# Kernel tuning notes

Measured on AMD Instinct MI355X. Metric: run time of the kernel, lower is better.

## Reference

```python
import jax, jax.numpy as jnp
import numpy as np

N = 50000   # nodes
E = 640000  # edges
D_IN = 128
D_OUT = 128
EPS = 1e-5


def _layer_norm(x, gamma, beta):
    mu = jnp.mean(x, axis=-1, keepdims=True)
    var = jnp.mean(jnp.square(x - mu), axis=-1, keepdims=True)
    return (x - mu) * jax.lax.rsqrt(var + EPS) * gamma + beta


def _sage_conv(x, src, dst, w_l, b_l, w_r):
    # PyG SAGEConv (aggr='mean', root_weight=True, normalize=False):
    #   out = lin_l(mean_{j in N(i)} x_j) + lin_r(x_i)
    msgs = x[src]                                             # [E, D]
    agg = jax.ops.segment_sum(msgs, dst, num_segments=N)      # [N, D]
    cnt = jax.ops.segment_sum(jnp.ones((E,), x.dtype), dst, num_segments=N)
    mean = agg / jnp.maximum(cnt, 1.0)[:, None]
    return mean @ w_l.T + b_l + x @ w_r.T


def setup_inputs() -> dict:
    key = jax.random.key(0)
    ks = jax.random.split(key, 12)
    s_in = 1.0 / np.sqrt(D_IN)
    s_out = 1.0 / np.sqrt(D_OUT)
    return {
        "x": jax.random.normal(ks[0], (N, D_IN), jnp.float32),
        "edges": jax.random.randint(ks[1], (2, E), 0, N),
        "dp_w": jax.random.uniform(ks[2], (D_OUT, D_IN), jnp.float32, -s_in, s_in),
        "dp_b": jnp.zeros((D_OUT,), jnp.float32),
        "sc_w": jax.random.uniform(ks[3], (D_OUT, D_IN), jnp.float32, -s_in, s_in),
        "sc_b": jnp.zeros((D_OUT,), jnp.float32),
        "g1_lw": jax.random.uniform(ks[4], (D_OUT, D_OUT), jnp.float32, -s_out, s_out),
        "g1_lb": jnp.zeros((D_OUT,), jnp.float32),
        "g1_rw": jax.random.uniform(ks[5], (D_OUT, D_OUT), jnp.float32, -s_out, s_out),
        "n1_g": jnp.ones((D_OUT,), jnp.float32),
        "n1_b": jnp.zeros((D_OUT,), jnp.float32),
        "g2_lw": jax.random.uniform(ks[6], (D_OUT, D_OUT), jnp.float32, -s_out, s_out),
        "g2_lb": jnp.zeros((D_OUT,), jnp.float32),
        "g2_rw": jax.random.uniform(ks[7], (D_OUT, D_OUT), jnp.float32, -s_out, s_out),
        "n2_g": jnp.ones((D_OUT,), jnp.float32),
        "n2_b": jnp.zeros((D_OUT,), jnp.float32),
    }


def reference(x, edges, dp_w, dp_b, sc_w, sc_b, g1_lw, g1_lb, g1_rw, n1_g, n1_b,
              g2_lw, g2_lb, g2_rw, n2_g, n2_b):
    gelu = lambda v: jax.nn.gelu(v, approximate=False)
    src, dst = edges[0], edges[1]
    shortcut = x @ sc_w.T + sc_b
    h = gelu(x @ dp_w.T + dp_b)
    h = _sage_conv(h, src, dst, g1_lw, g1_lb, g1_rw)
    h = gelu(_layer_norm(h, n1_g, n1_b))
    h = _sage_conv(h, src, dst, g2_lw, g2_lb, g2_rw)
    h = _layer_norm(h, n2_g, n2_b)
    return gelu(h + shortcut)
```

## Files before the change

kernel.cpp:

```cpp
#include <hip/hip_runtime.h>
#include <hip/hip_bf16.h>
#include <math.h>

#define D 128
#define WS 136
#define FS 132
#define PB 128

typedef __attribute__((ext_vector_type(8))) short bf16x8;
typedef __attribute__((ext_vector_type(4))) float f32x4;

__device__ __forceinline__ unsigned short f2bf(float f){
  return (unsigned short)((__float_as_uint(f) + 0x8000u) >> 16);
}
__device__ __forceinline__ float bf2f(unsigned short h){
  return __uint_as_float(((unsigned)h) << 16);
}
__device__ __forceinline__ float bf2f_lo(unsigned v){
  return __uint_as_float(v << 16);
}
__device__ __forceinline__ float bf2f_hi(unsigned v){
  return __uint_as_float(v & 0xFFFF0000u);
}
__device__ __forceinline__ float gelu_fast(float v){
  float u = v * v;
  float arg = v * (1.5957691216f + 0.0713548163f * u);
  arg = fminf(arg, 60.0f);
  float e = __expf(arg);
  return v * e * __builtin_amdgcn_rcpf(e + 1.0f);
}

__global__ __launch_bounds__(256) void k_prepcnt(const float* s0, const float* s1,
    const float* s2, const float* s3, const float* s4, const float* s5,
    unsigned short* dst, const int* __restrict__ edst, int* __restrict__ cnt,
    int E, int nbuck, int epb){
  __shared__ int hist[512];
  if (blockIdx.x < 48){
    int gt = blockIdx.x * 256 + threadIdx.x;
    int m = gt >> 11;
    int r = gt & 2047;
    int f = r >> 6, lane = r & 63;
    int t = f & 7, kk = f >> 3;
    int row = t * 16 + (lane & 15);
    int col = kk * 32 + (lane >> 4) * 8;
    const float* src;
    if (m == 0) src = s0; else if (m == 1) src = s1; else if (m == 2) src = s2;
    else if (m == 3) src = s3; else if (m == 4) src = s4; else src = s5;
    src += row * 128 + col;
    float4 a = *(const float4*)src;
    float4 bb = *(const float4*)(src + 4);
    bf16x8 o;
    o[0] = (short)f2bf(a.x);  o[1] = (short)f2bf(a.y);
    o[2] = (short)f2bf(a.z);  o[3] = (short)f2bf(a.w);
    o[4] = (short)f2bf(bb.x); o[5] = (short)f2bf(bb.y);
    o[6] = (short)f2bf(bb.z); o[7] = (short)f2bf(bb.w);
    int pair = m >> 1, half = m & 1;
    *(bf16x8*)(dst + (size_t)pair * 32768 + (((size_t)f * 2 + half) * 64 + lane) * 8) = o;
    return;
  }
  int blk = blockIdx.x - 48;
  for (int b = threadIdx.x; b < nbuck; b += 256) hist[b] = 0;
  __syncthreads();
  int start = blk * epb;
  int end = min(E, start + epb);
  for (int e = start + threadIdx.x; e < end; e += 256)
    atomicAdd(&hist[edst[e] >> 7], 1);
  __syncthreads();
  for (int b = threadIdx.x; b < nbuck; b += 256) cnt[blk * nbuck + b] = hist[b];
}

__global__ __launch_bounds__(256) void k_pscan(const int* __restrict__ cnt,
    int* __restrict__ offs, int* __restrict__ bbase, int E, int nbuck){
  __shared__ int tot[512], base[512];
  int t = threadIdx.x;
  for (int b = t; b < nbuck; b += 256){
    int s = 0;
    for (int blk = 0; blk < PB; blk++) s += cnt[blk * nbuck + b];
    tot[b] = s;
  }
  __syncthreads();
  for (int b = t; b < nbuck; b += 256){
    int s = 0;
    for (int j = 0; j < b; j++) s += tot[j];
    base[b] = s;
  }
  __syncthreads();
  for (int b = t; b < nbuck; b += 256){
    bbase[b] = base[b];
    int run = base[b];
    for (int blk = 0; blk < PB; blk++){
      offs[blk * nbuck + b] = run;
      run += cnt[blk * nbuck + b];
    }
  }
  if (t == 0) bbase[nbuck] = E;
}

__global__ __launch_bounds__(256) void k_pscatter(const int* __restrict__ esrc,
    const int* __restrict__ edst, const int* __restrict__ offs,
    unsigned* __restrict__ ebuf, int E, int nbuck, int epb){
  __shared__ int loff[512];
  for (int b = threadIdx.x; b < nbuck; b += 256) loff[b] = offs[blockIdx.x * nbuck + b];
  __syncthreads();
  int start = blockIdx.x * epb;
  int end = min(E, start + epb);
  for (int e = start + threadIdx.x; e < end; e += 256){
    int s = esrc[e], d = edst[e];
    int b = d >> 7;
    int pos = atomicAdd(&loff[b], 1);
    ebuf[pos] = (unsigned)s | ((unsigned)(d & 127) << 16);
  }
}

__global__ __launch_bounds__(256) void k_csrin(
    const unsigned* __restrict__ ebuf, const int* __restrict__ bbase,
    int* __restrict__ off, int* __restrict__ csr,
    const float* __restrict__ x, const unsigned short* __restrict__ wp,
    const float* __restrict__ scb, const float* __restrict__ dpb,
    unsigned short* __restrict__ sbuf, unsigned short* __restrict__ hbuf,
    int N, int E, int nbuck){
  __shared__ int cnt[128], pref[128], curs[128];
  __shared__ unsigned short tile[64 * WS];
  int tid = threadIdx.x;
  if ((int)blockIdx.x < nbuck){
    int b = blockIdx.x;
    int start = bbase[b], end = bbase[b + 1];
    if (tid < 128) cnt[tid] = 0;
    __syncthreads();
    for (int e = start + tid; e < end; e += 256)
      atomicAdd(&cnt[ebuf[e] >> 16], 1);
    __syncthreads();
    if (tid < 128) pref[tid] = cnt[tid];
    __syncthreads();
    for (int ofs = 1; ofs < 128; ofs <<= 1){
      int v = 0;
      if (tid < 128 && tid >= ofs) v = pref[tid - ofs];
      __syncthreads();
      if (tid < 128) pref[tid] += v;
      __syncthreads();
    }
    if (tid < 128){
      int ex = pref[tid] - cnt[tid];
      curs[tid] = ex;
      int node = b * 128 + tid;
      if (node < N) off[node] = start + ex;
    }
    if (b == 0 && tid == 0) off[N] = E;
    __syncthreads();
    for (int e = start + tid; e < end; e += 256){
      unsigned u = ebuf[e];
      int d = u >> 16;
      int p = atomicAdd(&curs[d], 1);
      csr[start + p] = (int)(u & 0xFFFFu);
    }
    return;
  }
  int bx = blockIdx.x - nbuck;
  int w = tid >> 6, lane = tid & 63, quad = lane >> 4, l16 = lane & 15;
  int nbb = bx * 64;
  int nb = nbb + w * 16;
  int arow = min(nb + l16, N - 1);
  f32x4 acc[2][8];
  #pragma unroll
  for (int m = 0; m < 2; m++)
    #pragma unroll
    for (int t = 0; t < 8; t++) acc[m][t] = (f32x4){0.f, 0.f, 0.f, 0.f};
  #pragma unroll
  for (int kk = 0; kk < 4; kk++){
    const float* xp = x + (size_t)arow * D + kk * 32 + quad * 8;
    float4 xa = *(const float4*)xp;
    float4 xb = *(const float4*)(xp + 4);
    bf16x8 a;
    a[0] = (short)f2bf(xa.x); a[1] = (short)f2bf(xa.y);
    a[2] = (short)f2bf(xa.z); a[3] = (short)f2bf(xa.w);
    a[4] = (short)f2bf(xb.x); a[5] = (short)f2bf(xb.y);
    a[6] = (short)f2bf(xb.z); a[7] = (short)f2bf(xb.w);
    #pragma unroll
    for (int t = 0; t < 8; t++){
      size_t fo = (((size_t)(kk * 8 + t) * 2) * 64 + lane) * 8;
      bf16x8 b0 = *(const bf16x8*)(wp + fo);
      bf16x8 b1 = *(const bf16x8*)(wp + fo + 512);
      acc[0][t] = __builtin_amdgcn_mfma_f32_16x16x32_bf16(a, b0, acc[0][t], 0, 0, 0);
      acc[1][t] = __builtin_amdgcn_mfma_f32_16x16x32_bf16(a, b1, acc[1][t], 0, 0, 0);
    }
  }
  #pragma unroll
  for (int m = 0; m < 2; m++){
    const float* bias = m ? dpb : scb;
    #pragma unroll
    for (int t = 0; t < 8; t++){
      float bv = bias[t * 16 + l16];
      #pragma unroll
      for (int r = 0; r < 4; r++){
        int nl = w * 16 + quad * 4 + r;
        float v = acc[m][t][r] + bv;
        if (m) v = gelu_fast(v);
        tile[nl * WS + t * 16 + l16] = f2bf(v);
      }
    }
    __syncthreads();
    unsigned short* dst = m ? hbuf : sbuf;
    #pragma unroll
    for (int i = 0; i < 4; i++){
      int c = tid + 256 * i;
      int nl = c >> 4, j = c & 15;
      int node = nbb + nl;
      if (node < N)
        *(bf16x8*)(dst + (size_t)node * D + j * 8) = *(const bf16x8*)(tile + nl * WS + j * 8);
    }
    __syncthreads();
  }
}

__global__ __launch_bounds__(256) void k_agg3(const unsigned short* __restrict__ h,
    const int* __restrict__ off, const int* __restrict__ csr,
    unsigned short* __restrict__ mbuf, int N){
  int tid = threadIdx.x;
  int wq = tid >> 4;
  int l16 = tid & 15;
  int base_node = blockIdx.x * 32 + wq * 2;
  float a[2][8];
  #pragma unroll
  for (int s = 0; s < 2; s++)
    #pragma unroll
    for (int c = 0; c < 8; c++) a[s][c] = 0.f;
  #pragma unroll
  for (int s = 0; s < 2; s++){
    int node = base_node + s;
    if (node < N){
      int e = off[node], e1 = off[node + 1];
      for (; e + 3 < e1; e += 4){
        int n0 = csr[e], n1 = csr[e + 1], n2 = csr[e + 2], n3 = csr[e + 3];
        uint4 v0 = *(const uint4*)(h + (size_t)n0 * D + l16 * 8);
        uint4 v1 = *(const uint4*)(h + (size_t)n1 * D + l16 * 8);
        uint4 v2 = *(const uint4*)(h + (size_t)n2 * D + l16 * 8);
        uint4 v3 = *(const uint4*)(h + (size_t)n3 * D + l16 * 8);
        a[s][0] += bf2f_lo(v0.x) + bf2f_lo(v1.x) + bf2f_lo(v2.x) + bf2f_lo(v3.x);
        a[s][1] += bf2f_hi(v0.x) + bf2f_hi(v1.x) + bf2f_hi(v2.x) + bf2f_hi(v3.x);
        a[s][2] += bf2f_lo(v0.y) + bf2f_lo(v1.y) + bf2f_lo(v2.y) + bf2f_lo(v3.y);
        a[s][3] += bf2f_hi(v0.y) + bf2f_hi(v1.y) + bf2f_hi(v2.y) + bf2f_hi(v3.y);
        a[s][4] += bf2f_lo(v0.z) + bf2f_lo(v1.z) + bf2f_lo(v2.z) + bf2f_lo(v3.z);
        a[s][5] += bf2f_hi(v0.z) + bf2f_hi(v1.z) + bf2f_hi(v2.z) + bf2f_hi(v3.z);
        a[s][6] += bf2f_lo(v0.w) + bf2f_lo(v1.w) + bf2f_lo(v2.w) + bf2f_lo(v3.w);
        a[s][7] += bf2f_hi(v0.w) + bf2f_hi(v1.w) + bf2f_hi(v2.w) + bf2f_hi(v3.w);
      }
      for (; e < e1; e++){
        int n0 = csr[e];
        uint4 v0 = *(const uint4*)(h + (size_t)n0 * D + l16 * 8);
        a[s][0] += bf2f_lo(v0.x); a[s][1] += bf2f_hi(v0.x);
        a[s][2] += bf2f_lo(v0.y); a[s][3] += bf2f_hi(v0.y);
        a[s][4] += bf2f_lo(v0.z); a[s][5] += bf2f_hi(v0.z);
        a[s][6] += bf2f_lo(v0.w); a[s][7] += bf2f_hi(v0.w);
      }
    }
  }
  #pragma unroll
  for (int s = 0; s < 2; s++){
    int node = base_node + s;
    if (node < N){
      int deg = off[node + 1] - off[node];
      float inv = 1.0f / (float)(deg > 1 ? deg : 1);
      uint4 o;
      o.x = ((unsigned)f2bf(a[s][1] * inv) << 16) | f2bf(a[s][0] * inv);
      o.y = ((unsigned)f2bf(a[s][3] * inv) << 16) | f2bf(a[s][2] * inv);
      o.z = ((unsigned)f2bf(a[s][5] * inv) << 16) | f2bf(a[s][4] * inv);
      o.w = ((unsigned)f2bf(a[s][7] * inv) << 16) | f2bf(a[s][6] * inv);
      *(uint4*)(mbuf + (size_t)node * D + l16 * 8) = o;
    }
  }
}

__global__ __launch_bounds__(256) void k_g(
    const unsigned short* __restrict__ hin, const unsigned short* __restrict__ mbuf,
    const unsigned short* __restrict__ wp,
    const float* __restrict__ lb, const float* __restrict__ gamma,
    const float* __restrict__ beta,
    const unsigned short* __restrict__ sbuf,
    unsigned short* __restrict__ hout, float* __restrict__ fout, int N, int mode){
  extern __shared__ char smraw[];
  unsigned short* stile = (unsigned short*)smraw;
  float* ftile = (float*)smraw;
  int tid = threadIdx.x, w = tid >> 6, lane = tid & 63, quad = lane >> 4, l16 = lane & 15;
  int nbb = blockIdx.x * 64;
  int nb = nbb + w * 16;
  int arow = min(nb + l16, N - 1);
  f32x4 acc[8];
  #pragma unroll
  for (int t = 0; t < 8; t++) acc[t] = (f32x4){0.f, 0.f, 0.f, 0.f};
  #pragma unroll
  for (int kk = 0; kk < 4; kk++){
    int co = kk * 32 + quad * 8;
    bf16x8 am = *(const bf16x8*)(mbuf + (size_t)arow * D + co);
    bf16x8 ah = *(const bf16x8*)(hin + (size_t)arow * D + co);
    #pragma unroll
    for (int t = 0; t < 8; t++){
      size_t fo = (((size_t)(kk * 8 + t) * 2) * 64 + lane) * 8;
      bf16x8 bl = *(const bf16x8*)(wp + fo);
      bf16x8 br = *(const bf16x8*)(wp + fo + 512);
      acc[t] = __builtin_amdgcn_mfma_f32_16x16x32_bf16(am, bl, acc[t], 0, 0, 0);
      acc[t] = __builtin_amdgcn_mfma_f32_16x16x32_bf16(ah, br, acc[t], 0, 0, 0);
    }
  }
  float lbv[8], gv[8], bv[8];
  #pragma unroll
  for (int t = 0; t < 8; t++){
    lbv[t] = lb[t * 16 + l16];
    gv[t] = gamma[t * 16 + l16];
    bv[t] = beta[t * 16 + l16];
  }
  float mu[4], rs[4];
  #pragma unroll
  for (int r = 0; r < 4; r++){
    float s = 0.f, qq = 0.f;
    #pragma unroll
    for (int t = 0; t < 8; t++){
      float v = acc[t][r] + lbv[t];
      acc[t][r] = v;
      s += v; qq += v * v;
    }
    s += __shfl_xor(s, 1); qq += __shfl_xor(qq, 1);
    s += __shfl_xor(s, 2); qq += __shfl_xor(qq, 2);
    s += __shfl_xor(s, 4); qq += __shfl_xor(qq, 4);
    s += __shfl_xor(s, 8); qq += __shfl_xor(qq, 8);
    float m_ = s * (1.f / 128.f);
    mu[r] = m_;
    rs[r] = rsqrtf(qq * (1.f / 128.f) - m_ * m_ + 1e-5f);
  }
  if (mode == 0){
    #pragma unroll
    for (int t = 0; t < 8; t++)
      #pragma unroll
      for (int r = 0; r < 4; r++){
        int nl = w * 16 + quad * 4 + r;
        float v = (acc[t][r] - mu[r]) * rs[r] * gv[t] + bv[t];
        stile[nl * WS + t * 16 + l16] = f2bf(gelu_fast(v));
      }
    __syncthreads();
    #pragma unroll
    for (int i = 0; i < 4; i++){
      int c = tid + 256 * i;
      int nl = c >> 4, j = c & 15;
      int node = nbb + nl;
      if (node < N)
        *(bf16x8*)(hout + (size_t)node * D + j * 8) = *(const bf16x8*)(stile + nl * WS + j * 8);
    }
  } else {
    #pragma unroll
    for (int i = 0; i < 4; i++){
      int c = tid + 256 * i;
      int nl = c >> 4, j = c & 15;
      int node = nbb + nl;
      bf16x8 v = (bf16x8){0,0,0,0,0,0,0,0};
      if (node < N) v = *(const bf16x8*)(sbuf + (size_t)node * D + j * 8);
      *(bf16x8*)(stile + nl * WS + j * 8) = v;
    }
    __syncthreads();
    float sc[8][4];
    #pragma unroll
    for (int t = 0; t < 8; t++)
      #pragma unroll
      for (int r = 0; r < 4; r++){
        int nl = w * 16 + quad * 4 + r;
        sc[t][r] = bf2f(stile[nl * WS + t * 16 + l16]);
      }
    __syncthreads();
    #pragma unroll
    for (int t = 0; t < 8; t++)
      #pragma unroll
      for (int r = 0; r < 4; r++){
        int nl = w * 16 + quad * 4 + r;
        float v = (acc[t][r] - mu[r]) * rs[r] * gv[t] + bv[t];
        ftile[nl * FS + t * 16 + l16] = gelu_fast(v + sc[t][r]);
      }
    __syncthreads();
    #pragma unroll
    for (int i = 0; i < 8; i++){
      int c = tid + 256 * i;
      int nl = c >> 5, j = c & 31;
      int node = nbb + nl;
      if (node < N)
        *(float4*)(fout + (size_t)node * D + j * 4) = *(const float4*)(ftile + nl * FS + j * 4);
    }
  }
}

extern "C" void kernel_launch(void* const* d_in, const int* in_sizes, int n_in,
                              void* d_out, int out_size, void* d_ws, size_t ws_size,
                              hipStream_t stream){
  const float* x     = (const float*)d_in[0];
  const int*   edges = (const int*)d_in[1];
  const float* dp_w  = (const float*)d_in[2];
  const float* dp_b  = (const float*)d_in[3];
  const float* sc_w  = (const float*)d_in[4];
  const float* sc_b  = (const float*)d_in[5];
  const float* g1_lw = (const float*)d_in[6];
  const float* g1_lb = (const float*)d_in[7];
  const float* g1_rw = (const float*)d_in[8];
  const float* n1_g  = (const float*)d_in[9];
  const float* n1_b  = (const float*)d_in[10];
  const float* g2_lw = (const float*)d_in[11];
  const float* g2_lb = (const float*)d_in[12];
  const float* g2_rw = (const float*)d_in[13];
  const float* n2_g  = (const float*)d_in[14];
  const float* n2_b  = (const float*)d_in[15];

  const int N = in_sizes[0] / D;
  const int E = in_sizes[1] / 2;
  const int* esrc = edges;
  const int* edst = edges + E;
  const int nbuck = (N + 127) >> 7;
  const int epb = (E + PB - 1) / PB;

  char* base = (char*)d_ws;
  size_t cur = 0;
  auto carve = [&](size_t b) -> char* {
    char* p = base + cur;
    cur = (cur + b + 255) & ~(size_t)255;
    return p;
  };
  unsigned* ebuf = (unsigned*)carve((size_t)E * 4);
  int* cnt       = (int*)carve((size_t)PB * nbuck * 4);
  int* offs      = (int*)carve((size_t)PB * nbuck * 4);
  int* bbase     = (int*)carve((size_t)(nbuck + 1) * 4);
  int* off       = (int*)carve((size_t)(N + 1) * 4);
  int* csr       = (int*)carve((size_t)E * 4);
  unsigned short* wb    = (unsigned short*)carve((size_t)3 * 32768 * 2);
  unsigned short* hbuf  = (unsigned short*)carve((size_t)N * D * 2);
  unsigned short* h1buf = (unsigned short*)carve((size_t)N * D * 2);
  unsigned short* mbuf  = (unsigned short*)carve((size_t)N * D * 2);
  unsigned short* sbuf  = (unsigned short*)carve((size_t)N * D * 2);

  unsigned short* wp0 = wb;
  unsigned short* wp1 = wb + 32768;
  unsigned short* wp2 = wb + 2 * 32768;

  float* out = (float*)d_out;

  k_prepcnt<<<48 + PB, 256, 0, stream>>>(sc_w, dp_w, g1_lw, g1_rw, g2_lw, g2_rw,
                                         wb, edst, cnt, E, nbuck, epb);
  k_pscan<<<1, 256, 0, stream>>>(cnt, offs, bbase, E, nbuck);
  k_pscatter<<<PB, 256, 0, stream>>>(esrc, edst, offs, ebuf, E, nbuck, epb);

  const int nin = (N + 63) / 64;
  k_csrin<<<nbuck + nin, 256, 0, stream>>>(ebuf, bbase, off, csr,
                                           x, wp0, sc_b, dp_b, sbuf, hbuf,
                                           N, E, nbuck);

  const int nagg = (N + 31) / 32;
  k_agg3<<<nagg, 256, 0, stream>>>(hbuf, off, csr, mbuf, N);
  k_g<<<nin, 256, 17408, stream>>>(hbuf, mbuf, wp1, g1_lb, n1_g, n1_b,
                                   nullptr, h1buf, nullptr, N, 0);
  k_agg3<<<nagg, 256, 0, stream>>>(h1buf, off, csr, mbuf, N);
  k_g<<<nin, 256, 33792, stream>>>(h1buf, mbuf, wp2, g2_lb, n2_g, n2_b,
                                   sbuf, nullptr, out, N, 1);
}
```

Before: 248.1 us.

## Parallelize bucket prefix scan across blocks and batch gather over node pairs

Replaces the single-block serial k_pscan with a per-bucket parallel scan kernel (k_scanA), and moves the cross-bucket exclusive prefix into k_pscatter and k_csrin, which each recompute it from bucket totals. The goal is to remove a serial single-block bottleneck in CSR construction. The aggregation kernel now walks the combined edge range of two adjacent nodes in batches of eight, prefetching the next batch's indices, and splits the sums with masked accumulators. This gives more memory-level parallelism per thread but adds redundant masked FMAs and a subtraction that may introduce small rounding differences.

```diff
diff --git a/kernel.cpp b/kernel.cpp
--- a/kernel.cpp
+++ b/kernel.cpp
@@ -69,38 +69,35 @@
   for (int b = threadIdx.x; b < nbuck; b += 256) cnt[blk * nbuck + b] = hist[b];
 }
 
-__global__ __launch_bounds__(256) void k_pscan(const int* __restrict__ cnt,
-    int* __restrict__ offs, int* __restrict__ bbase, int E, int nbuck){
-  __shared__ int tot[512], base[512];
-  int t = threadIdx.x;
-  for (int b = t; b < nbuck; b += 256){
+__global__ __launch_bounds__(128) void k_scanA(const int* __restrict__ cnt,
+    int* __restrict__ offs_rel, int* __restrict__ tot, int nbuck){
+  __shared__ int sm[128];
+  int b = blockIdx.x, t = threadIdx.x;
+  int v = cnt[t * nbuck + b];
+  sm[t] = v; __syncthreads();
+  for (int ofs = 1; ofs < 128; ofs <<= 1){
+    int u = (t >= ofs) ? sm[t - ofs] : 0;
+    __syncthreads();
+    sm[t] += u;
+    __syncthreads();
+  }
+  offs_rel[t * nbuck + b] = sm[t] - v;
+  if (t == 127) tot[b] = sm[127];
+}
+
+__global__ __launch_bounds__(256) void k_pscatter(const int* __restrict__ esrc,
+    const int* __restrict__ edst, const int* __restrict__ offs_rel,
+    const int* __restrict__ tot, unsigned* __restrict__ ebuf,
+    int E, int nbuck, int epb){
+  __shared__ int stot[512];
+  __shared__ int loff[512];
+  for (int b = threadIdx.x; b < nbuck; b += 256) stot[b] = tot[b];
+  __syncthreads();
+  for (int b = threadIdx.x; b < nbuck; b += 256){
     int s = 0;
-    for (int blk = 0; blk < PB; blk++) s += cnt[blk * nbuck + b];
-    tot[b] = s;
-  }
-  __syncthreads();
-  for (int b = t; b < nbuck; b += 256){
-    int s = 0;
-    for (int j = 0; j < b; j++) s += tot[j];
-    base[b] = s;
-  }
-  __syncthreads();
-  for (int b = t; b < nbuck; b += 256){
-    bbase[b] = base[b];
-    int run = base[b];
-    for (int blk = 0; blk < PB; blk++){
-      offs[blk * nbuck + b] = run;
-      run += cnt[blk * nbuck + b];
-    }
-  }
-  if (t == 0) bbase[nbuck] = E;
-}
-
-__global__ __launch_bounds__(256) void k_pscatter(const int* __restrict__ esrc,
-    const int* __restrict__ edst, const int* __restrict__ offs,
-    unsigned* __restrict__ ebuf, int E, int nbuck, int epb){
-  __shared__ int loff[512];
-  for (int b = threadIdx.x; b < nbuck; b += 256) loff[b] = offs[blockIdx.x * nbuck + b];
+    for (int j = 0; j < b; j++) s += stot[j];
+    loff[b] = s + offs_rel[blockIdx.x * nbuck + b];
+  }
   __syncthreads();
   int start = blockIdx.x * epb;
   int end = min(E, start + epb);
@@ -113,18 +110,30 @@
 }
 
 __global__ __launch_bounds__(256) void k_csrin(
-    const unsigned* __restrict__ ebuf, const int* __restrict__ bbase,
+    const unsigned* __restrict__ ebuf, const int* __restrict__ tot,
     int* __restrict__ off, int* __restrict__ csr,
     const float* __restrict__ x, const unsigned short* __restrict__ wp,
     const float* __restrict__ scb, const float* __restrict__ dpb,
     unsigned short* __restrict__ sbuf, unsigned short* __restrict__ hbuf,
     int N, int E, int nbuck){
   __shared__ int cnt[128], pref[128], curs[128];
+  __shared__ int stot[512], red[256];
   __shared__ unsigned short tile[64 * WS];
   int tid = threadIdx.x;
   if ((int)blockIdx.x < nbuck){
     int b = blockIdx.x;
-    int start = bbase[b], end = bbase[b + 1];
+    for (int j = tid; j < nbuck; j += 256) stot[j] = tot[j];
+    __syncthreads();
+    int part = 0;
+    for (int j = tid; j < b; j += 256) part += stot[j];
+    red[tid] = part;
+    __syncthreads();
+    for (int ofs = 128; ofs > 0; ofs >>= 1){
+      if (tid < ofs) red[tid] += red[tid + ofs];
+      __syncthreads();
+    }
+    int start = red[0];
+    int end = start + stot[b];
     if (tid < 128) cnt[tid] = 0;
     __syncthreads();
     for (int e = start + tid; e < end; e += 256)
@@ -218,55 +227,60 @@
   int tid = threadIdx.x;
   int wq = tid >> 4;
   int l16 = tid & 15;
-  int base_node = blockIdx.x * 32 + wq * 2;
-  float a[2][8];
-  #pragma unroll
-  for (int s = 0; s < 2; s++)
-    #pragma unroll
-    for (int c = 0; c < 8; c++) a[s][c] = 0.f;
-  #pragma unroll
-  for (int s = 0; s < 2; s++){
-    int node = base_node + s;
-    if (node < N){
-      int e = off[node], e1 = off[node + 1];
-      for (; e + 3 < e1; e += 4){
-        int n0 = csr[e], n1 = csr[e + 1], n2 = csr[e + 2], n3 = csr[e + 3];
-        uint4 v0 = *(const uint4*)(h + (size_t)n0 * D + l16 * 8);
-        uint4 v1 = *(const uint4*)(h + (size_t)n1 * D + l16 * 8);
-        uint4 v2 = *(const uint4*)(h + (size_t)n2 * D + l16 * 8);
-        uint4 v3 = *(const uint4*)(h + (size_t)n3 * D + l16 * 8);
-        a[s][0] += bf2f_lo(v0.x) + bf2f_lo(v1.x) + bf2f_lo(v2.x) + bf2f_lo(v3.x);
-        a[s][1] += bf2f_hi(v0.x) + bf2f_hi(v1.x) + bf2f_hi(v2.x) + bf2f_hi(v3.x);
-        a[s][2] += bf2f_lo(v0.y) + bf2f_lo(v1.y) + bf2f_lo(v2.y) + bf2f_lo(v3.y);
-        a[s][3] += bf2f_hi(v0.y) + bf2f_hi(v1.y) + bf2f_hi(v2.y) + bf2f_hi(v3.y);
-        a[s][4] += bf2f_lo(v0.z) + bf2f_lo(v1.z) + bf2f_lo(v2.z) + bf2f_lo(v3.z);
-        a[s][5] += bf2f_hi(v0.z) + bf2f_hi(v1.z) + bf2f_hi(v2.z) + bf2f_hi(v3.z);
-        a[s][6] += bf2f_lo(v0.w) + bf2f_lo(v1.w) + bf2f_lo(v2.w) + bf2f_lo(v3.w);
-        a[s][7] += bf2f_hi(v0.w) + bf2f_hi(v1.w) + bf2f_hi(v2.w) + bf2f_hi(v3.w);
+  int n0 = blockIdx.x * 32 + wq * 2;
+  if (n0 >= N) return;
+  int n1v = (n0 + 1 < N);
+  int s0 = off[n0];
+  int split = off[n0 + 1];
+  int e1 = n1v ? off[n0 + 2] : split;
+  float aall[8], ahi[8];
+  #pragma unroll
+  for (int c = 0; c < 8; c++){ aall[c] = 0.f; ahi[c] = 0.f; }
+  if (e1 > s0){
+    int nn[8];
+    #pragma unroll
+    for (int i = 0; i < 8; i++) nn[i] = csr[min(s0 + i, e1 - 1)];
+    for (int e = s0; e < e1; e += 8){
+      uint4 v[8];
+      #pragma unroll
+      for (int i = 0; i < 8; i++)
+        v[i] = *(const uint4*)(h + (size_t)nn[i] * D + l16 * 8);
+      #pragma unroll
+      for (int i = 0; i < 8; i++) nn[i] = csr[min(e + 8 + i, e1 - 1)];
+      #pragma unroll
+      for (int i = 0; i < 8; i++){
+        float mv = (e + i < e1) ? 1.f : 0.f;
+        float mh = (e + i >= split) ? mv : 0.f;
+        aall[0] += mv * bf2f_lo(v[i].x); ahi[0] += mh * bf2f_lo(v[i].x);
+        aall[1] += mv * bf2f_hi(v[i].x); ahi[1] += mh * bf2f_hi(v[i].x);
+        aall[2] += mv * bf2f_lo(v[i].y); ahi[2] += mh * bf2f_lo(v[i].y);
+        aall[3] += mv * bf2f_hi(v[i].y); ahi[3] += mh * bf2f_hi(v[i].y);
+        aall[4] += mv * bf2f_lo(v[i].z); ahi[4] += mh * bf2f_lo(v[i].z);
+        aall[5] += mv * bf2f_hi(v[i].z); ahi[5] += mh * bf2f_hi(v[i].z);
+        aall[6] += mv * bf2f_lo(v[i].w); ahi[6] += mh * bf2f_lo(v[i].w);
+        aall[7] += mv * bf2f_hi(v[i].w); ahi[7] += mh * bf2f_hi(v[i].w);
       }
-      for (; e < e1; e++){
-        int n0 = csr[e];
-        uint4 v0 = *(const uint4*)(h + (size_t)n0 * D + l16 * 8);
-        a[s][0] += bf2f_lo(v0.x); a[s][1] += bf2f_hi(v0.x);
-        a[s][2] += bf2f_lo(v0.y); a[s][3] += bf2f_hi(v0.y);
-        a[s][4] += bf2f_lo(v0.z); a[s][5] += bf2f_hi(v0.z);
-        a[s][6] += bf2f_lo(v0.w); a[s][7] += bf2f_hi(v0.w);
-      }
-    }
-  }
-  #pragma unroll
-  for (int s = 0; s < 2; s++){
-    int node = base_node + s;
-    if (node < N){
-      int deg = off[node + 1] - off[node];
-      float inv = 1.0f / (float)(deg > 1 ? deg : 1);
-      uint4 o;
-      o.x = ((unsigned)f2bf(a[s][1] * inv) << 16) | f2bf(a[s][0] * inv);
-      o.y = ((unsigned)f2bf(a[s][3] * inv) << 16) | f2bf(a[s][2] * inv);
-      o.z = ((unsigned)f2bf(a[s][5] * inv) << 16) | f2bf(a[s][4] * inv);
-      o.w = ((unsigned)f2bf(a[s][7] * inv) << 16) | f2bf(a[s][6] * inv);
-      *(uint4*)(mbuf + (size_t)node * D + l16 * 8) = o;
-    }
+    }
+  }
+  {
+    int deg0 = split - s0;
+    float inv = 1.0f / (float)(deg0 > 1 ? deg0 : 1);
+    uint4 o;
+    o.x = ((unsigned)f2bf((aall[1] - ahi[1]) * inv) << 16) | f2bf((aall[0] - ahi[0]) * inv);
+    o.y = ((unsigned)f2bf((aall[3] - ahi[3]) * inv) << 16) | f2bf((aall[2] - ahi[2]) * inv);
+    o.z = ((unsigned)f2bf((aall[5] - ahi[5]) * inv) << 16) | f2bf((aall[4] - ahi[4]) * inv);
+    o.w = ((unsigned)f2bf((aall[7] - ahi[7]) * inv) << 16) | f2bf((aall[6] - ahi[6]) * inv);
+    *(uint4*)(mbuf + (size_t)n0 * D + l16 * 8) = o;
+  }
+  if (n1v){
+    int deg1 = e1 - split;
+    float inv = 1.0f / (float)(deg1 > 1 ? deg1 : 1);
+    uint4 o;
+    o.x = ((unsigned)f2bf(ahi[1] * inv) << 16) | f2bf(ahi[0] * inv);
+    o.y = ((unsigned)f2bf(ahi[3] * inv) << 16) | f2bf(ahi[2] * inv);
+    o.z = ((unsigned)f2bf(ahi[5] * inv) << 16) | f2bf(ahi[4] * inv);
+    o.w = ((unsigned)f2bf(ahi[7] * inv) << 16) | f2bf(ahi[6] * inv);
+    *(uint4*)(mbuf + (size_t)(n0 + 1) * D + l16 * 8) = o;
   }
 }
 
@@ -418,12 +432,12 @@
     cur = (cur + b + 255) & ~(size_t)255;
     return p;
   };
-  unsigned* ebuf = (unsigned*)carve((size_t)E * 4);
-  int* cnt       = (int*)carve((size_t)PB * nbuck * 4);
-  int* offs      = (int*)carve((size_t)PB * nbuck * 4);
-  int* bbase     = (int*)carve((size_t)(nbuck + 1) * 4);
-  int* off       = (int*)carve((size_t)(N + 1) * 4);
-  int* csr       = (int*)carve((size_t)E * 4);
+  unsigned* ebuf  = (unsigned*)carve((size_t)E * 4);
+  int* cnt        = (int*)carve((size_t)PB * nbuck * 4);
+  int* offs_rel   = (int*)carve((size_t)PB * nbuck * 4);
+  int* tot        = (int*)carve((size_t)nbuck * 4);
+  int* off        = (int*)carve((size_t)(N + 1) * 4);
+  int* csr        = (int*)carve((size_t)E * 4);
   unsigned short* wb    = (unsigned short*)carve((size_t)3 * 32768 * 2);
   unsigned short* hbuf  = (unsigned short*)carve((size_t)N * D * 2);
   unsigned short* h1buf = (unsigned short*)carve((size_t)N * D * 2);
@@ -438,11 +452,11 @@
 
   k_prepcnt<<<48 + PB, 256, 0, stream>>>(sc_w, dp_w, g1_lw, g1_rw, g2_lw, g2_rw,
                                          wb, edst, cnt, E, nbuck, epb);
-  k_pscan<<<1, 256, 0, stream>>>(cnt, offs, bbase, E, nbuck);
-  k_pscatter<<<PB, 256, 0, stream>>>(esrc, edst, offs, ebuf, E, nbuck, epb);
+  k_scanA<<<nbuck, 128, 0, stream>>>(cnt, offs_rel, tot, nbuck);
+  k_pscatter<<<PB, 256, 0, stream>>>(esrc, edst, offs_rel, tot, ebuf, E, nbuck, epb);
 
   const int nin = (N + 63) / 64;
-  k_csrin<<<nbuck + nin, 256, 0, stream>>>(ebuf, bbase, off, csr,
+  k_csrin<<<nbuck + nin, 256, 0, stream>>>(ebuf, tot, off, csr,
                                            x, wp0, sc_b, dp_b, sbuf, hbuf,
                                            N, E, nbuck);
 
```

Result: no change. 248.7 us (+0.2%).
